# Kernel optimization log

Hardware: AMD Instinct MI355X
Metric: run time of the kernel (lower is better)

Reference implementation:

```python
import jax, jax.numpy as jnp
import numpy as np

DIM = 512
HEADS = 8
DHEAD = 64
INNER = HEADS * DHEAD
GAMMA = 0.01
LAMBDA_REG = 0.001


def _ln(x, g, b, eps=1e-5):
    mu = x.mean(-1, keepdims=True)
    var = jnp.var(x, axis=-1, keepdims=True)
    return (x - mu) / jnp.sqrt(var + eps) * g + b


def setup_inputs() -> dict:
    key = jax.random.key(0)
    ks = jax.random.split(key, 16)
    B, NQ, NK = 4, 1024, 1024
    s = 0.02
    return {
        "q": jax.random.normal(ks[0], (B, NQ, DIM), jnp.float32),
        "k": jax.random.normal(ks[1], (B, NK, DIM), jnp.float32),
        "v": jax.random.normal(ks[2], (B, NK, DIM), jnp.float32),
        "ln_g": jnp.ones((DIM,), jnp.float32),
        "ln_b": jnp.zeros((DIM,), jnp.float32),
        "W_in": jax.random.normal(ks[3], (DIM, INNER), jnp.float32) * s,
        "wp_W1": jax.random.normal(ks[4], (2 * DHEAD, 3 * DHEAD), jnp.float32) * s,
        "wp_b1": jnp.zeros((3 * DHEAD,), jnp.float32),
        "wp_lng": jnp.ones((3 * DHEAD,), jnp.float32),
        "wp_lnb": jnp.zeros((3 * DHEAD,), jnp.float32),
        "wp_W2": jax.random.normal(ks[5], (3 * DHEAD, 2 * DHEAD), jnp.float32) * s,
        "wp_b2": jnp.zeros((2 * DHEAD,), jnp.float32),
        "wp_W3": jax.random.normal(ks[6], (2 * DHEAD, 3), jnp.float32) * s,
        "wp_b3": jnp.zeros((3,), jnp.float32),
        "w_temp": jnp.array(1.8, jnp.float32),
        "W_out": jax.random.normal(ks[7], (INNER, DIM), jnp.float32) * s,
        "b_out": jnp.zeros((DIM,), jnp.float32),
    }


def _forward(q, k, v, ln_g, ln_b, W_in, wp_W1, wp_b1, wp_lng, wp_lnb,
             wp_W2, wp_b2, wp_W3, wp_b3, w_temp, W_out, b_out):
    h, d = HEADS, DHEAD
    sg = jax.lax.stop_gradient

    def proj(x):
        f = _ln(x, ln_g, ln_b) @ W_in               # [B,N,inner] (dropout: eval)
        B, N, _ = f.shape
        return f.reshape(B, N, h, d).transpose(2, 0, 1, 3)  # [h,B,N,d]

    f_q, f_k, f_v = proj(q), proj(k), proj(v)
    m = f_k.shape[2]
    eps = 1e-8

    # --- cosine_distance(f_q, f_k^T), clamped twice in original ---
    dots0 = jnp.einsum('hbnd,hbmd->hbnm', f_q, f_k)
    n1 = jnp.linalg.norm(f_q, axis=-1, keepdims=True) + eps      # [h,B,N,1]
    n2 = jnp.linalg.norm(f_k, axis=-1, keepdims=True) + eps      # [h,B,M,1]
    cosine_sim = jnp.clip(dots0 / (n1 * n2.transpose(0, 1, 3, 2)), -0.98, 0.98)

    # --- regularized covariance component ---
    f_k_c = f_k - f_k.mean(axis=2, keepdims=True)
    f_q_c = f_q - f_q.mean(axis=-1, keepdims=True)
    cov = jnp.einsum('hbnd,hbmd->hbnm', f_q_c, f_k_c) / (d ** 0.5 + 1e-6)
    health = sg(jnp.std(cov, ddof=1))
    base = LAMBDA_REG / m
    reg = jnp.where(health < 1e-5, base * 8.0,
                    jnp.where(health < 1e-3, base * 3.0, base))
    cov = jnp.clip(reg * cov, -30.0, 30.0)

    # --- margin-based variance component (eval: adaptive_gamma = gamma) ---
    fq_n = f_q / jnp.maximum(jnp.linalg.norm(f_q, axis=-1, keepdims=True), 1e-6)
    fk_n = f_k / jnp.maximum(jnp.linalg.norm(f_k, axis=-1, keepdims=True), 1e-6)
    cs = jnp.clip(jnp.einsum('hbnd,hbmd->hbnm', fq_n, fk_n), -0.98, 0.98)
    margin = jnp.clip(GAMMA - cs, 0.0, 8.0)
    var_c = jnp.broadcast_to(margin.mean(-1, keepdims=True), cs.shape)

    # --- dynamic per-head weights ---
    feat = jnp.concatenate([f_q.mean(axis=(1, 2)), f_k.mean(axis=(1, 2))], -1)  # [h,2d]
    hid = jax.nn.relu(_ln(feat @ wp_W1 + wp_b1, wp_lng, wp_lnb))
    hid = jax.nn.relu(hid @ wp_W2 + wp_b2)
    probs = jax.nn.softmax(hid @ wp_W3 + wp_b3, axis=-1)   # predictor ends in softmax
    wt = jnp.clip(w_temp, 0.05, 3.0)
    w = jax.nn.softmax(probs / wt, axis=-1)                # second softmax, per original
    w = jnp.clip(w, 0.05, 0.85)
    w = w / w.sum(-1, keepdims=True)
    cw = w[:, 0][:, None, None, None]
    covw = w[:, 1][:, None, None, None]
    varw = w[:, 2][:, None, None, None]

    cos_norm = sg(jnp.std(cosine_sim, ddof=1)) + 1e-6
    cov_norm = sg(jnp.std(cov, ddof=1)) + 1e-6
    var_norm = sg(jnp.std(var_c, ddof=1)) + 1e-6
    cos_h = jnp.minimum(cos_norm, 1.2)
    cov_h = jnp.minimum(cov_norm * 12.0, 1.2)
    var_h = jnp.minimum(var_norm * 12.0, 1.2)

    dots = (cw * (cosine_sim / cos_norm * cos_h)
            + covw * (cov / cov_norm * 0.5 * cov_h)
            + varw * (var_c / var_norm * 0.5 * var_h))

    div = sg(jnp.std(dots, ddof=1))
    temp = jnp.where(div < 5e-6, 0.03, jnp.where(div < 5e-4, 0.15, 0.4))
    attn = jax.nn.softmax(dots / temp, axis=-1)
    out = jnp.einsum('hbnm,hbmd->hbnd', attn, f_v)
    out = out.transpose(1, 2, 0, 3).reshape(q.shape[0], q.shape[1], h * d)
    return out @ W_out + b_out


def reference(q, k, v, ln_g, ln_b, W_in, wp_W1, wp_b1, wp_lng, wp_lnb,
              wp_W2, wp_b2, wp_W3, wp_b3, w_temp, W_out, b_out):
    return _forward(q, k, v, ln_g, ln_b, W_in, wp_W1, wp_b1, wp_lng, wp_lnb,
                    wp_W2, wp_b2, wp_W3, wp_b3, w_temp, W_out, b_out)
```

## Files before the change

### kernel.cpp

```cpp
#include <hip/hip_runtime.h>
#include <math.h>

#define SZ 2097152

typedef __attribute__((ext_vector_type(8))) short bf16x8;
typedef __attribute__((ext_vector_type(4))) float f32x4;
#define MFMA16(A,B,C) __builtin_amdgcn_mfma_f32_16x16x32_bf16(A,B,C,0,0,0)

__device__ __forceinline__ unsigned short f2b(float x) {
  unsigned int u = __float_as_uint(x);
  u = (u + 0x7fffu + ((u >> 16) & 1u)) >> 16;
  return (unsigned short)u;
}
__device__ __forceinline__ unsigned int pk2(float a, float b) {
  return (unsigned int)f2b(a) | ((unsigned int)f2b(b) << 16);
}
#define B2FL(u) __uint_as_float(((unsigned)(u)) << 16)
#define B2FH(u) __uint_as_float(((unsigned)(u)) & 0xffff0000u)

__device__ __forceinline__ float wredsum(float v) {
  #pragma unroll
  for (int o = 32; o; o >>= 1) v += __shfl_xor(v, o);
  return v;
}

__device__ __forceinline__ int swz(int r, int c) { return (r << 6) + ((c ^ (r & 7)) << 3); }

__device__ __forceinline__ bf16x8 ldfrag(const unsigned short* s, int row, int chunk) {
  return *reinterpret_cast<const bf16x8*>(&s[swz(row, chunk)]);
}

__device__ __forceinline__ void gl16(const unsigned short* g, unsigned short* l) {
  __builtin_amdgcn_global_load_lds(
      (const __attribute__((address_space(1))) void*)g,
      (__attribute__((address_space(3))) void*)l, 16, 0, 0);
}

__global__ __launch_bounds__(256) void k_pre(
    const float* __restrict__ q, const float* __restrict__ k, const float* __restrict__ v,
    const float* __restrict__ ln_g, const float* __restrict__ ln_b,
    const float* __restrict__ Win, const float* __restrict__ Wout,
    unsigned short* __restrict__ A_bf, unsigned short* __restrict__ WT,
    double* __restrict__ stats)
{
  __shared__ float t[64][65];
  const int bx = blockIdx.x;
  const int tid = threadIdx.x;
  if (bx < 128) {
    const int x = bx & 63;
    const int k0 = (x & 7) << 6, n0 = (x >> 3) << 6;
    const float* W = (bx >> 6) ? Wout : Win;
    unsigned short* dst = WT + (size_t)(bx >> 6) * 262144;
    for (int u = tid; u < 4096; u += 256) {
      const int r = u >> 6, c = u & 63;
      t[c][r] = W[(size_t)(k0 + r) * 512 + n0 + c];
    }
    __syncthreads();
    for (int u = tid; u < 4096; u += 256) {
      const int r = u >> 6, c = u & 63;
      dst[(size_t)(n0 + r) * 512 + k0 + c] = f2b(t[r][c]);
    }
    return;
  }
  if (bx == 3200) {
    if (tid < 72) stats[tid] = 0.0;
    return;
  }
  const int wv = tid >> 6, lane = tid & 63;
  const int row = (bx - 128) * 4 + wv;
  const int tt = row >> 12, g = row & 4095;
  const float* x = (tt == 0) ? q : (tt == 1) ? k : v;
  const float4* xr = reinterpret_cast<const float4*>(x + (size_t)g * 512);
  const float4 a0 = xr[2 * lane], a1 = xr[2 * lane + 1];
  float s  = a0.x + a0.y + a0.z + a0.w + a1.x + a1.y + a1.z + a1.w;
  float ss = a0.x*a0.x + a0.y*a0.y + a0.z*a0.z + a0.w*a0.w
           + a1.x*a1.x + a1.y*a1.y + a1.z*a1.z + a1.w*a1.w;
  #pragma unroll
  for (int o = 32; o; o >>= 1) { s += __shfl_xor(s, o); ss += __shfl_xor(ss, o); }
  const float mu = s * (1.f / 512.f);
  const float rstd = rsqrtf(ss * (1.f / 512.f) - mu * mu + 1e-5f);
  const float4* gg = reinterpret_cast<const float4*>(ln_g);
  const float4* bb = reinterpret_cast<const float4*>(ln_b);
  const float4 g0 = gg[2 * lane], g1 = gg[2 * lane + 1];
  const float4 b0 = bb[2 * lane], b1 = bb[2 * lane + 1];
  uint4 o4;
  o4.x = pk2((a0.x - mu) * rstd * g0.x + b0.x, (a0.y - mu) * rstd * g0.y + b0.y);
  o4.y = pk2((a0.z - mu) * rstd * g0.z + b0.z, (a0.w - mu) * rstd * g0.w + b0.w);
  o4.z = pk2((a1.x - mu) * rstd * g1.x + b1.x, (a1.y - mu) * rstd * g1.y + b1.y);
  o4.w = pk2((a1.z - mu) * rstd * g1.z + b1.z, (a1.w - mu) * rstd * g1.w + b1.w);
  *reinterpret_cast<uint4*>(&A_bf[(size_t)row * 512 + lane * 8]) = o4;
}

__global__ __launch_bounds__(256) void k_projcol(
    const unsigned short* __restrict__ A_bf, const unsigned short* __restrict__ WT,
    unsigned short* __restrict__ BF, float* __restrict__ partialA)
{
  __shared__ __align__(16) unsigned short smem[12288];
  const int tid = threadIdx.x;
  if (blockIdx.x >= 192) {
    const int u0 = (blockIdx.x - 192) * 4 + blockIdx.y;
    const int t = u0 >> 6, seg = u0 & 63;
    const unsigned int* src = reinterpret_cast<const unsigned int*>(
        A_bf + ((size_t)t * 4096 + seg * 64) * 512);
    float s0 = 0.f, s1 = 0.f;
    #pragma unroll 4
    for (int r = 0; r < 64; ++r) {
      const unsigned int vv = src[r * 256 + tid];
      s0 += B2FL(vv);
      s1 += B2FH(vv);
    }
    partialA[(((size_t)t * 64 + seg) << 9) + tid * 2] = s0;
    partialA[(((size_t)t * 64 + seg) << 9) + tid * 2 + 1] = s1;
    return;
  }
  unsigned short* As = smem;
  unsigned short* Bs = smem + 4096;
  const int m0 = blockIdx.x * 64;
  const int n0b = blockIdx.y * 128;
  const int w = tid >> 6, lane = tid & 63;
  const int wm = w >> 1, wn = w & 1;
  const int lr = lane & 15, lg = lane >> 4;
  f32x4 acc[2][4];
  #pragma unroll
  for (int mi = 0; mi < 2; ++mi)
    #pragma unroll
    for (int ni = 0; ni < 4; ++ni) acc[mi][ni] = f32x4{0.f, 0.f, 0.f, 0.f};

  for (int k0 = 0; k0 < 512; k0 += 64) {
    __syncthreads();
    #pragma unroll
    for (int p = 0; p < 2; ++p) {
      const int u = p * 256 + w * 64 + lane;
      const int r = u >> 3, cs = (u & 7) ^ (r & 7);
      gl16(&A_bf[(size_t)(m0 + r) * 512 + k0 + cs * 8], &As[(size_t)u * 8]);
    }
    #pragma unroll
    for (int p = 0; p < 4; ++p) {
      const int u = p * 256 + w * 64 + lane;
      const int r = u >> 3, cs = (u & 7) ^ (r & 7);
      gl16(&WT[(size_t)(n0b + r) * 512 + k0 + cs * 8], &Bs[(size_t)u * 8]);
    }
    __syncthreads();
    bf16x8 a[2][2];
    #pragma unroll
    for (int mi = 0; mi < 2; ++mi) {
      const int ar = wm * 32 + mi * 16 + lr;
      a[mi][0] = ldfrag(As, ar, lg);
      a[mi][1] = ldfrag(As, ar, 4 + lg);
    }
    #pragma unroll
    for (int ni = 0; ni < 4; ++ni) {
      const int br = wn * 64 + ni * 16 + lr;
      const bf16x8 b0 = ldfrag(Bs, br, lg);
      const bf16x8 b1 = ldfrag(Bs, br, 4 + lg);
      acc[0][ni] = MFMA16(a[0][0], b0, acc[0][ni]);
      acc[0][ni] = MFMA16(a[0][1], b1, acc[0][ni]);
      acc[1][ni] = MFMA16(a[1][0], b0, acc[1][ni]);
      acc[1][ni] = MFMA16(a[1][1], b1, acc[1][ni]);
    }
  }
  const int t = m0 >> 12;
  const int gmb = (m0 & 4095) + wm * 32;
  const int h = 2 * blockIdx.y + wn;
  if (t < 2) {
    #pragma unroll
    for (int mi = 0; mi < 2; ++mi) {
      #pragma unroll
      for (int reg = 0; reg < 4; ++reg) {
        float ss = 0.f;
        #pragma unroll
        for (int ni = 0; ni < 4; ++ni) { const float vv = acc[mi][ni][reg]; ss += vv * vv; }
        #pragma unroll
        for (int o = 1; o < 16; o <<= 1) ss += __shfl_xor(ss, o);
        const float inv = 1.f / (sqrtf(ss) + 1e-8f);
        const int g = gmb + mi * 16 + lg * 4 + reg;
        const int b = g >> 10, n = g & 1023;
        const size_t base = (size_t)t * SZ + ((((size_t)(h * 4 + b) << 10) | n) << 6);
        #pragma unroll
        for (int ni = 0; ni < 4; ++ni) {
          BF[base + ni * 16 + lr] = f2b(acc[mi][ni][reg] * inv);
        }
      }
    }
  } else {
    unsigned short* FVT = BF + (size_t)2 * SZ;
    __syncthreads();
    #pragma unroll
    for (int mi = 0; mi < 2; ++mi)
      #pragma unroll
      for (int ni = 0; ni < 4; ++ni)
        #pragma unroll
        for (int reg = 0; reg < 4; ++reg)
          smem[(wn * 64 + ni * 16 + lr) * 66 + (wm * 32 + mi * 16 + lg * 4 + reg)] =
              f2b(acc[mi][ni][reg]);
    __syncthreads();
    const int gv0 = m0 & 4095;
    const int b = gv0 >> 10, nb = gv0 & 1023;
    for (int u = tid; u < 4096; u += 256) {
      const int jl = u >> 5, nl = (u & 31) << 1;
      const int h2 = 2 * blockIdx.y + (jl >> 6), d = jl & 63;
      const unsigned int vv = *reinterpret_cast<const unsigned int*>(&smem[jl * 66 + nl]);
      *reinterpret_cast<unsigned int*>(
          &FVT[((size_t)(h2 * 4 + b) << 16) + d * 1024 + nb + nl]) = vv;
    }
  }
}

__global__ __launch_bounds__(256) void k_mid(const unsigned short* __restrict__ BF,
                                             const float* __restrict__ partialA,
                                             const unsigned short* __restrict__ WT,
                                             double* __restrict__ stats,
                                             float* __restrict__ feats)
{
  __shared__ __align__(16) unsigned short kn_s[4096];
  __shared__ float part[5][4];
  __shared__ float mean_s[512];
  const int tid = threadIdx.x;
  if (blockIdx.x >= 32) {
    const int t = blockIdx.x - 32;
    float a0 = 0.f, a1 = 0.f;
    #pragma unroll 8
    for (int s = 0; s < 64; ++s) {
      a0 += partialA[(((size_t)t * 64 + s) << 9) + tid * 2];
      a1 += partialA[(((size_t)t * 64 + s) << 9) + tid * 2 + 1];
    }
    mean_s[tid * 2] = a0 * (1.f / 4096.f);
    mean_s[tid * 2 + 1] = a1 * (1.f / 4096.f);
    __syncthreads();
    #pragma unroll
    for (int uu = 0; uu < 2; ++uu) {
      const int j = tid * 2 + uu;
      const unsigned short* wr = WT + (size_t)j * 512;
      float a = 0.f;
      for (int kk = 0; kk < 512; ++kk) a += mean_s[kk] * B2FL(wr[kk]);
      feats[t * 512 + j] = a;
    }
    return;
  }
  const int pair = blockIdx.x, h = pair >> 2;
  const int w = tid >> 6, lane = tid & 63;
  const int lr = lane & 15, lg = lane >> 4;
  const size_t pb = (size_t)pair * 65536;
  const unsigned short* fqn = BF + pb;
  const unsigned short* fkn = BF + (size_t)SZ + pb;

  const int qrow = w * 16 + lr;
  const unsigned short* qnp = fqn + (size_t)qrow * 64;
  const bf16x8 qn0 = *reinterpret_cast<const bf16x8*>(qnp + lg * 8);
  const bf16x8 qn1 = *reinterpret_cast<const bf16x8*>(qnp + 32 + lg * 8);

  float sx = 0.f, sxx = 0.f;
  float rxs[4] = {0, 0, 0, 0}, rms[4] = {0, 0, 0, 0};

  for (int m0 = 0; m0 < 1024; m0 += 64) {
    __syncthreads();
    #pragma unroll
    for (int p = 0; p < 2; ++p) {
      const int u = p * 256 + w * 64 + lane;
      const int r = u >> 3, cs = (u & 7) ^ (r & 7);
      gl16(&fkn[((size_t)(m0 + r) << 6) + cs * 8], &kn_s[(size_t)u * 8]);
    }
    __syncthreads();
    #pragma unroll
    for (int nt = 0; nt < 4; ++nt) {
      const int krow = nt * 16 + lr;
      f32x4 dn = {0.f, 0.f, 0.f, 0.f};
      dn = MFMA16(qn0, ldfrag(kn_s, krow, lg), dn);
      dn = MFMA16(qn1, ldfrag(kn_s, krow, 4 + lg), dn);
      #pragma unroll
      for (int r = 0; r < 4; ++r) {
        const float X = fminf(fmaxf(dn[r], -0.98f), 0.98f);
        sx += X; sxx += X * X;
        rxs[r] += X; rms[r] += fmaxf(0.01f - X, 0.f);
      }
    }
  }
  const float g0 = wredsum(sx), g1 = wredsum(sxx);
  #pragma unroll
  for (int r = 0; r < 4; ++r) {
    #pragma unroll
    for (int o = 1; o < 16; o <<= 1) {
      rxs[r] += __shfl_xor(rxs[r], o);
      rms[r] += __shfl_xor(rms[r], o);
    }
  }
  float z1 = 0.f, z2 = 0.f, z3 = 0.f;
  if (lr == 0) {
    #pragma unroll
    for (int r = 0; r < 4; ++r) {
      const float Z = rms[r] * (1.f / 1024.f);
      z1 += Z; z2 += Z * Z; z3 += Z * rxs[r];
    }
  }
  z1 = wredsum(z1); z2 = wredsum(z2); z3 = wredsum(z3);
  if (lane == 0) {
    part[0][w] = g0; part[1][w] = g1; part[2][w] = z1; part[3][w] = z2; part[4][w] = z3;
  }
  __syncthreads();
  if (tid == 0) {
    const int dst[5] = {0, 1, 5, 6, 7};
    #pragma unroll
    for (int i = 0; i < 5; ++i) {
      const double s = (double)part[i][0] + part[i][1] + part[i][2] + part[i][3];
      atomicAdd(&stats[h * 9 + dst[i]], s);
    }
  }
}

__global__ __launch_bounds__(512) void k_finalize(
    const float* __restrict__ feats, const double* __restrict__ stats,
    const float* __restrict__ W1, const float* __restrict__ b1,
    const float* __restrict__ lng, const float* __restrict__ lnb,
    const float* __restrict__ W2, const float* __restrict__ b2,
    const float* __restrict__ W3, const float* __restrict__ b3,
    const float* __restrict__ w_temp, float* __restrict__ coefs)
{
  __shared__ float feat[8][128];
  __shared__ float h1[8][192];
  __shared__ float y2[8][128];
  __shared__ float wsm[8][3];
  const int tid = threadIdx.x;
  const int h = tid >> 6, lane = tid & 63;

  feat[h][lane] = feats[h * 64 + lane];
  feat[h][64 + lane] = feats[512 + h * 64 + lane];
  float y1v[3];
  {
    float a0 = b1[lane], a1 = b1[lane + 64], a2 = b1[lane + 128];
    for (int i = 0; i < 128; ++i) {
      const float fv = feat[h][i];
      const float* wr = W1 + (size_t)i * 192;
      a0 += fv * wr[lane];
      a1 += fv * wr[lane + 64];
      a2 += fv * wr[lane + 128];
    }
    y1v[0] = a0; y1v[1] = a1; y1v[2] = a2;
  }
  float s = y1v[0] + y1v[1] + y1v[2];
  float ss = y1v[0]*y1v[0] + y1v[1]*y1v[1] + y1v[2]*y1v[2];
  s = wredsum(s); ss = wredsum(ss);
  const float mu = s * (1.f / 192.f);
  const float rstd = rsqrtf(ss * (1.f / 192.f) - mu * mu + 1e-5f);
  #pragma unroll
  for (int u = 0; u < 3; ++u) {
    const int j = lane + u * 64;
    h1[h][j] = fmaxf((y1v[u] - mu) * rstd * lng[j] + lnb[j], 0.f);
  }
  {
    float a0 = b2[lane], a1 = b2[lane + 64];
    for (int i = 0; i < 192; ++i) {
      const float hv = h1[h][i];
      const float* wr = W2 + (size_t)i * 128;
      a0 += hv * wr[lane];
      a1 += hv * wr[lane + 64];
    }
    y2[h][lane] = fmaxf(a0, 0.f);
    y2[h][lane + 64] = fmaxf(a1, 0.f);
  }
  {
    float l0, l1, l2;
    const float va = y2[h][lane], vb = y2[h][lane + 64];
    const float* wa = W3 + (size_t)lane * 3;
    const float* wb = W3 + (size_t)(lane + 64) * 3;
    l0 = va * wa[0] + vb * wb[0];
    l1 = va * wa[1] + vb * wb[1];
    l2 = va * wa[2] + vb * wb[2];
    l0 = wredsum(l0); l1 = wredsum(l1); l2 = wredsum(l2);
    if (lane == 0) {
      l0 += b3[0]; l1 += b3[1]; l2 += b3[2];
      float mx = fmaxf(l0, fmaxf(l1, l2));
      float e0 = expf(l0 - mx), e1 = expf(l1 - mx), e2 = expf(l2 - mx);
      float se = e0 + e1 + e2;
      const float p0 = e0 / se, p1 = e1 / se, p2 = e2 / se;
      const float wt = fminf(fmaxf(w_temp[0], 0.05f), 3.f);
      const float q0 = p0 / wt, q1 = p1 / wt, q2 = p2 / wt;
      mx = fmaxf(q0, fmaxf(q1, q2));
      e0 = expf(q0 - mx); e1 = expf(q1 - mx); e2 = expf(q2 - mx);
      se = e0 + e1 + e2;
      float w0 = e0 / se, w1 = e1 / se, w2 = e2 / se;
      w0 = fminf(fmaxf(w0, 0.05f), 0.85f);
      w1 = fminf(fmaxf(w1, 0.05f), 0.85f);
      w2 = fminf(fmaxf(w2, 0.05f), 0.85f);
      const float swt = w0 + w1 + w2;
      wsm[h][0] = w0 / swt; wsm[h][1] = w1 / swt; wsm[h][2] = w2 / swt;
    }
  }
  __syncthreads();
  if (tid == 0) {
    const double n = 2097152.0, M = 1024.0;
    const double L2E = 1.4426950408889634;
    double S[8][9], T[9];
    for (int i = 0; i < 9; ++i) T[i] = 0.0;
    for (int hh = 0; hh < 8; ++hh)
      for (int i = 0; i < 9; ++i) { S[hh][i] = stats[hh * 9 + i]; T[i] += S[hh][i]; }
    const double cos_norm = sqrt(fmax((T[1] - T[0] * T[0] / n) / (n - 1.0), 0.0)) + 1e-6;
    const double zvar = (M * T[6] - (M * T[5]) * (M * T[5]) / n) / (n - 1.0);
    const double var_norm = sqrt(fmax(zvar, 0.0)) + 1e-6;
    const double cos_h = fmin(cos_norm, 1.2);
    const double var_h = fmin(var_norm * 12.0, 1.2);
    double D1 = 0.0, D2 = 0.0, Ah[8];
    for (int hh = 0; hh < 8; ++hh) {
      const double A = (double)wsm[hh][0] * cos_h / cos_norm;
      const double C = (double)wsm[hh][2] * 0.5 * var_h / var_norm;
      Ah[hh] = A;
      D1 += A * S[hh][0] + C * M * S[hh][5];
      D2 += A * A * S[hh][1] + C * C * M * S[hh][6] + 2.0 * A * C * S[hh][7];
    }
    const double divv = sqrt(fmax((D2 - D1 * D1 / n) / (n - 1.0), 0.0));
    const double temp = (divv < 5e-6) ? 0.03 : ((divv < 5e-4) ? 0.15 : 0.4);
    for (int hh = 0; hh < 8; ++hh) {
      const float Pp = (float)(Ah[hh] / temp * L2E);
      coefs[hh] = Pp;
      coefs[16 + hh] = fabsf(Pp) * 0.98f;
    }
  }
}

__global__ __launch_bounds__(256) void k_attn(const unsigned short* __restrict__ BF,
                                              const float* __restrict__ coefs,
                                              unsigned short* __restrict__ po,
                                              float* __restrict__ pl)
{
  __shared__ __align__(16) unsigned short kn_s[4096], vt_s[4096], P_s[4096];
  const int pair = blockIdx.y, h = pair >> 2, seg = blockIdx.z;
  const int r0 = blockIdx.x * 64;
  const int tid = threadIdx.x;
  const int w = tid >> 6, lane = tid & 63;
  const int lr = lane & 15, lg = lane >> 4;
  const size_t pb = (size_t)pair * 65536;
  const unsigned short* fqn = BF + pb;
  const unsigned short* fkn = BF + (size_t)SZ + pb;
  const unsigned short* fvt = BF + (size_t)2 * SZ + pb;
  const float P = coefs[h], MB = coefs[16 + h];

  const int qrow = r0 + w * 16 + lr;
  const unsigned short* qnp = fqn + (size_t)qrow * 64;
  const bf16x8 qn0 = *reinterpret_cast<const bf16x8*>(qnp + lg * 8);
  const bf16x8 qn1 = *reinterpret_cast<const bf16x8*>(qnp + 32 + lg * 8);

  float lsum = 0.f;
  f32x4 o[4];
  #pragma unroll
  for (int i = 0; i < 4; ++i) o[i] = f32x4{0.f, 0.f, 0.f, 0.f};

  const int qb = w * 16 + lr;
  const int pofs = 4 * (lg & 1);
  const int chi = lg >> 1;

  const int mbeg = seg << 9;
  for (int m0 = mbeg; m0 < mbeg + 512; m0 += 64) {
    __syncthreads();
    #pragma unroll
    for (int p = 0; p < 2; ++p) {
      const int u = p * 256 + w * 64 + lane;
      const int r = u >> 3, cs = (u & 7) ^ (r & 7);
      gl16(&fkn[((size_t)(m0 + r) << 6) + cs * 8], &kn_s[(size_t)u * 8]);
      gl16(&fvt[(size_t)r * 1024 + m0 + cs * 8], &vt_s[(size_t)u * 8]);
    }
    __syncthreads();

    __builtin_amdgcn_s_setprio(1);
    #pragma unroll
    for (int nt = 0; nt < 4; ++nt) {
      const int krow = nt * 16 + lr;
      f32x4 dn = {0.f, 0.f, 0.f, 0.f};
      dn = MFMA16(ldfrag(kn_s, krow, lg), qn0, dn);
      dn = MFMA16(ldfrag(kn_s, krow, 4 + lg), qn1, dn);
      float e[4];
      #pragma unroll
      for (int r = 0; r < 4; ++r) {
        const float X = fminf(fmaxf(dn[r], -0.98f), 0.98f);
        e[r] = exp2f(P * X - MB);
        lsum += e[r];
      }
      unsigned int w0, w1;
      asm("v_cvt_pk_bf16_f32 %0, %1, %2" : "=v"(w0) : "v"(e[0]), "v"(e[1]));
      asm("v_cvt_pk_bf16_f32 %0, %1, %2" : "=v"(w1) : "v"(e[2]), "v"(e[3]));
      const int chunk = 2 * nt + chi;
      *reinterpret_cast<uint2*>(
          &P_s[(qb << 6) + ((chunk ^ (qb & 7)) << 3) + pofs]) = uint2{w0, w1};
    }
    const int parow = w * 16 + lr;
    const bf16x8 pa0 = ldfrag(P_s, parow, lg);
    const bf16x8 pa1 = ldfrag(P_s, parow, 4 + lg);
    #pragma unroll
    for (int nt2 = 0; nt2 < 4; ++nt2) {
      const int vrow = nt2 * 16 + lr;
      o[nt2] = MFMA16(pa0, ldfrag(vt_s, vrow, lg), o[nt2]);
      o[nt2] = MFMA16(pa1, ldfrag(vt_s, vrow, 4 + lg), o[nt2]);
    }
    __builtin_amdgcn_s_setprio(0);
  }
  lsum += __shfl_xor(lsum, 16);
  lsum += __shfl_xor(lsum, 32);
  const size_t sb = (size_t)seg * SZ;
  #pragma unroll
  for (int r = 0; r < 4; ++r) {
    const int lrow = w * 16 + 4 * lg + r;
    const size_t orow = sb + pb + ((size_t)(r0 + lrow) << 6);
    #pragma unroll
    for (int nt2 = 0; nt2 < 4; ++nt2) {
      po[orow + nt2 * 16 + lr] = f2b(o[nt2][r]);
    }
  }
  if (lg == 0) {
    pl[(seg << 15) + pair * 1024 + r0 + w * 16 + lr] = lsum;
  }
}

__global__ __launch_bounds__(256) void k_gemm_out(
    const unsigned short* __restrict__ po, const float* __restrict__ pl,
    const unsigned short* __restrict__ WT,
    const float* __restrict__ bias, float* __restrict__ out)
{
  __shared__ __align__(16) unsigned short As[2048], Bs[8192];
  __shared__ float sinv_s[256];
  const int m0 = blockIdx.x * 32;
  const int n0b = blockIdx.y * 128;
  const int tid = threadIdx.x;
  const int w = tid >> 6, lane = tid & 63;
  const int wm = w >> 1, wn = w & 1;
  const int lr = lane & 15, lg = lane >> 4;
  {
    const int r2 = tid >> 3, h2 = tid & 7;
    const int g2 = m0 + r2;
    const int rowid = (h2 * 4 + (g2 >> 10)) * 1024 + (g2 & 1023);
    sinv_s[tid] = 1.f / (pl[rowid] + pl[32768 + rowid]);
  }
  f32x4 acc[4];
  #pragma unroll
  for (int ni = 0; ni < 4; ++ni) acc[ni] = f32x4{0.f, 0.f, 0.f, 0.f};

  for (int k0 = 0; k0 < 512; k0 += 64) {
    __syncthreads();
    {
      const int r = tid >> 3, c = tid & 7;
      const int g = m0 + r;
      const int j0 = k0 + c * 8;
      const int h = k0 >> 6;
      const size_t base = ((size_t)(h * 4 + (g >> 10)) << 16) + ((size_t)(g & 1023) << 6) + (j0 & 63);
      const uint4 v0 = *reinterpret_cast<const uint4*>(po + base);
      const uint4 v1 = *reinterpret_cast<const uint4*>(po + (size_t)SZ + base);
      const float sv = sinv_s[r * 8 + h];
      uint4 o4;
      o4.x = pk2((B2FL(v0.x) + B2FL(v1.x)) * sv, (B2FH(v0.x) + B2FH(v1.x)) * sv);
      o4.y = pk2((B2FL(v0.y) + B2FL(v1.y)) * sv, (B2FH(v0.y) + B2FH(v1.y)) * sv);
      o4.z = pk2((B2FL(v0.z) + B2FL(v1.z)) * sv, (B2FH(v0.z) + B2FH(v1.z)) * sv);
      o4.w = pk2((B2FL(v0.w) + B2FL(v1.w)) * sv, (B2FH(v0.w) + B2FH(v1.w)) * sv);
      *reinterpret_cast<uint4*>(&As[swz(r, c)]) = o4;
    }
    #pragma unroll
    for (int p = 0; p < 4; ++p) {
      const int u = p * 256 + w * 64 + lane;
      const int r = u >> 3, cs = (u & 7) ^ (r & 7);
      gl16(&WT[(size_t)(n0b + r) * 512 + k0 + cs * 8], &Bs[(size_t)u * 8]);
    }
    __syncthreads();
    const int ar = wm * 16 + lr;
    const bf16x8 a0 = ldfrag(As, ar, lg);
    const bf16x8 a1 = ldfrag(As, ar, 4 + lg);
    #pragma unroll
    for (int ni = 0; ni < 4; ++ni) {
      const int br = wn * 64 + ni * 16 + lr;
      const bf16x8 b0 = ldfrag(Bs, br, lg);
      const bf16x8 b1 = ldfrag(Bs, br, 4 + lg);
      acc[ni] = MFMA16(a0, b0, acc[ni]);
      acc[ni] = MFMA16(a1, b1, acc[ni]);
    }
  }
  #pragma unroll
  for (int ni = 0; ni < 4; ++ni) {
    const int j = n0b + wn * 64 + ni * 16 + lr;
    const float bj = bias[j];
    #pragma unroll
    for (int reg = 0; reg < 4; ++reg) {
      const int g = m0 + wm * 16 + lg * 4 + reg;
      out[(size_t)g * 512 + j] = acc[ni][reg] + bj;
    }
  }
}

extern "C" void kernel_launch(void* const* d_in, const int* in_sizes, int n_in,
                              void* d_out, int out_size, void* d_ws, size_t ws_size,
                              hipStream_t stream) {
  (void)in_sizes; (void)n_in; (void)out_size; (void)ws_size;
  const float* q      = (const float*)d_in[0];
  const float* k      = (const float*)d_in[1];
  const float* v      = (const float*)d_in[2];
  const float* ln_g   = (const float*)d_in[3];
  const float* ln_b   = (const float*)d_in[4];
  const float* W_in   = (const float*)d_in[5];
  const float* wp_W1  = (const float*)d_in[6];
  const float* wp_b1  = (const float*)d_in[7];
  const float* wp_lng = (const float*)d_in[8];
  const float* wp_lnb = (const float*)d_in[9];
  const float* wp_W2  = (const float*)d_in[10];
  const float* wp_b2  = (const float*)d_in[11];
  const float* wp_W3  = (const float*)d_in[12];
  const float* wp_b3  = (const float*)d_in[13];
  const float* w_temp = (const float*)d_in[14];
  const float* W_out  = (const float*)d_in[15];
  const float* b_out  = (const float*)d_in[16];

  float* ws = (float*)d_ws;
  unsigned short* BF = (unsigned short*)ws;
  unsigned short* A_bf = BF + (size_t)3 * SZ;
  unsigned short* po = (unsigned short*)(ws + (size_t)3 * SZ / 2);
  float* AUX  = ws + (size_t)13631488;
  float* feats  = AUX;
  float* coefs = AUX + 4096;
  double* stats = (double*)(AUX + 4160);
  unsigned short* WT = (unsigned short*)(AUX + 8192);
  float* partialA = AUX + 270336;
  float* pl = AUX + 8192;

  k_pre<<<3201, 256, 0, stream>>>(q, k, v, ln_g, ln_b, W_in, W_out, A_bf, WT, stats);
  k_projcol<<<dim3(224, 4), 256, 0, stream>>>(A_bf, WT, BF, partialA);
  k_mid<<<34, 256, 0, stream>>>(BF, partialA, WT, stats, feats);
  k_finalize<<<1, 512, 0, stream>>>(feats, stats, wp_W1, wp_b1, wp_lng, wp_lnb,
                                    wp_W2, wp_b2, wp_W3, wp_b3, w_temp, coefs);
  k_attn<<<dim3(16, 32, 2), 256, 0, stream>>>(BF, coefs, po, pl);
  k_gemm_out<<<dim3(128, 4), 256, 0, stream>>>(po, pl, WT + 262144, b_out, (float*)d_out);
}
```

Before: 95.91 us.

## Double-buffer LDS tiles in projection, attention and output GEMM kernels

Result: slower. 100.5 us (+4.8%).

```diff
diff --git a/kernel.cpp b/kernel.cpp
--- a/kernel.cpp
+++ b/kernel.cpp
@@ -95,7 +95,7 @@
     const unsigned short* __restrict__ A_bf, const unsigned short* __restrict__ WT,
     unsigned short* __restrict__ BF, float* __restrict__ partialA)
 {
-  __shared__ __align__(16) unsigned short smem[12288];
+  __shared__ __align__(16) unsigned short smem[24576];
   const int tid = threadIdx.x;
   if (blockIdx.x >= 192) {
     const int u0 = (blockIdx.x - 192) * 4 + blockIdx.y;
@@ -113,8 +113,6 @@
     partialA[(((size_t)t * 64 + seg) << 9) + tid * 2 + 1] = s1;
     return;
   }
-  unsigned short* As = smem;
-  unsigned short* Bs = smem + 4096;
   const int m0 = blockIdx.x * 64;
   const int n0b = blockIdx.y * 128;
   const int w = tid >> 6, lane = tid & 63;
@@ -126,21 +124,41 @@
     #pragma unroll
     for (int ni = 0; ni < 4; ++ni) acc[mi][ni] = f32x4{0.f, 0.f, 0.f, 0.f};
 
-  for (int k0 = 0; k0 < 512; k0 += 64) {
-    __syncthreads();
-    #pragma unroll
-    for (int p = 0; p < 2; ++p) {
-      const int u = p * 256 + w * 64 + lane;
-      const int r = u >> 3, cs = (u & 7) ^ (r & 7);
-      gl16(&A_bf[(size_t)(m0 + r) * 512 + k0 + cs * 8], &As[(size_t)u * 8]);
-    }
-    #pragma unroll
-    for (int p = 0; p < 4; ++p) {
-      const int u = p * 256 + w * 64 + lane;
-      const int r = u >> 3, cs = (u & 7) ^ (r & 7);
-      gl16(&WT[(size_t)(n0b + r) * 512 + k0 + cs * 8], &Bs[(size_t)u * 8]);
-    }
-    __syncthreads();
+  #pragma unroll
+  for (int p = 0; p < 2; ++p) {
+    const int u = p * 256 + w * 64 + lane;
+    const int r = u >> 3, cs = (u & 7) ^ (r & 7);
+    gl16(&A_bf[(size_t)(m0 + r) * 512 + cs * 8], &smem[(size_t)u * 8]);
+  }
+  #pragma unroll
+  for (int p = 0; p < 4; ++p) {
+    const int u = p * 256 + w * 64 + lane;
+    const int r = u >> 3, cs = (u & 7) ^ (r & 7);
+    gl16(&WT[(size_t)(n0b + r) * 512 + cs * 8], &smem[8192 + (size_t)u * 8]);
+  }
+  __syncthreads();
+  int cur = 0;
+  for (int kt = 0; kt < 8; ++kt) {
+    if (kt < 7) {
+      const int k0 = (kt + 1) * 64;
+      const int nb = (cur ^ 1);
+      #pragma unroll
+      for (int p = 0; p < 2; ++p) {
+        const int u = p * 256 + w * 64 + lane;
+        const int r = u >> 3, cs = (u & 7) ^ (r & 7);
+        gl16(&A_bf[(size_t)(m0 + r) * 512 + k0 + cs * 8],
+             &smem[nb * 4096 + (size_t)u * 8]);
+      }
+      #pragma unroll
+      for (int p = 0; p < 4; ++p) {
+        const int u = p * 256 + w * 64 + lane;
+        const int r = u >> 3, cs = (u & 7) ^ (r & 7);
+        gl16(&WT[(size_t)(n0b + r) * 512 + k0 + cs * 8],
+             &smem[8192 + nb * 8192 + (size_t)u * 8]);
+      }
+    }
+    const unsigned short* As = smem + cur * 4096;
+    const unsigned short* Bs = smem + 8192 + cur * 8192;
     bf16x8 a[2][2];
     #pragma unroll
     for (int mi = 0; mi < 2; ++mi) {
@@ -148,6 +166,7 @@
       a[mi][0] = ldfrag(As, ar, lg);
       a[mi][1] = ldfrag(As, ar, 4 + lg);
     }
+    __builtin_amdgcn_s_setprio(1);
     #pragma unroll
     for (int ni = 0; ni < 4; ++ni) {
       const int br = wn * 64 + ni * 16 + lr;
@@ -158,6 +177,9 @@
       acc[1][ni] = MFMA16(a[1][0], b0, acc[1][ni]);
       acc[1][ni] = MFMA16(a[1][1], b1, acc[1][ni]);
     }
+    __builtin_amdgcn_s_setprio(0);
+    __syncthreads();
+    cur ^= 1;
   }
   const int t = m0 >> 12;
   const int gmb = (m0 & 4095) + wm * 32;
@@ -184,7 +206,6 @@
     }
   } else {
     unsigned short* FVT = BF + (size_t)2 * SZ;
-    __syncthreads();
     #pragma unroll
     for (int mi = 0; mi < 2; ++mi)
       #pragma unroll
@@ -421,7 +442,7 @@
                                               unsigned short* __restrict__ po,
                                               float* __restrict__ pl)
 {
-  __shared__ __align__(16) unsigned short kn_s[4096], vt_s[4096], P_s[4096];
+  __shared__ __align__(16) unsigned short kn_s[2][4096], vt_s[2][4096], P_s[4096];
   const int pair = blockIdx.y, h = pair >> 2, seg = blockIdx.z;
   const int r0 = blockIdx.x * 64;
   const int tid = threadIdx.x;
@@ -446,26 +467,37 @@
   const int qb = w * 16 + lr;
   const int pofs = 4 * (lg & 1);
   const int chi = lg >> 1;
-
   const int mbeg = seg << 9;
-  for (int m0 = mbeg; m0 < mbeg + 512; m0 += 64) {
-    __syncthreads();
-    #pragma unroll
-    for (int p = 0; p < 2; ++p) {
-      const int u = p * 256 + w * 64 + lane;
-      const int r = u >> 3, cs = (u & 7) ^ (r & 7);
-      gl16(&fkn[((size_t)(m0 + r) << 6) + cs * 8], &kn_s[(size_t)u * 8]);
-      gl16(&fvt[(size_t)r * 1024 + m0 + cs * 8], &vt_s[(size_t)u * 8]);
-    }
-    __syncthreads();
-
+
+  #pragma unroll
+  for (int p = 0; p < 2; ++p) {
+    const int u = p * 256 + w * 64 + lane;
+    const int r = u >> 3, cs = (u & 7) ^ (r & 7);
+    gl16(&fkn[((size_t)(mbeg + r) << 6) + cs * 8], &kn_s[0][(size_t)u * 8]);
+    gl16(&fvt[(size_t)r * 1024 + mbeg + cs * 8], &vt_s[0][(size_t)u * 8]);
+  }
+  __syncthreads();
+  int cur = 0;
+  for (int ti = 0; ti < 8; ++ti) {
+    if (ti < 7) {
+      const int m0 = mbeg + (ti + 1) * 64;
+      #pragma unroll
+      for (int p = 0; p < 2; ++p) {
+        const int u = p * 256 + w * 64 + lane;
+        const int r = u >> 3, cs = (u & 7) ^ (r & 7);
+        gl16(&fkn[((size_t)(m0 + r) << 6) + cs * 8], &kn_s[cur ^ 1][(size_t)u * 8]);
+        gl16(&fvt[(size_t)r * 1024 + m0 + cs * 8], &vt_s[cur ^ 1][(size_t)u * 8]);
+      }
+    }
+    const unsigned short* kc = kn_s[cur];
+    const unsigned short* vc = vt_s[cur];
     __builtin_amdgcn_s_setprio(1);
     #pragma unroll
     for (int nt = 0; nt < 4; ++nt) {
       const int krow = nt * 16 + lr;
       f32x4 dn = {0.f, 0.f, 0.f, 0.f};
-      dn = MFMA16(ldfrag(kn_s, krow, lg), qn0, dn);
-      dn = MFMA16(ldfrag(kn_s, krow, 4 + lg), qn1, dn);
+      dn = MFMA16(ldfrag(kc, krow, lg), qn0, dn);
+      dn = MFMA16(ldfrag(kc, krow, 4 + lg), qn1, dn);
       float e[4];
       #pragma unroll
       for (int r = 0; r < 4; ++r) {
@@ -486,10 +518,12 @@
     #pragma unroll
     for (int nt2 = 0; nt2 < 4; ++nt2) {
       const int vrow = nt2 * 16 + lr;
-      o[nt2] = MFMA16(pa0, ldfrag(vt_s, vrow, lg), o[nt2]);
-      o[nt2] = MFMA16(pa1, ldfrag(vt_s, vrow, 4 + lg), o[nt2]);
+      o[nt2] = MFMA16(pa0, ldfrag(vc, vrow, lg), o[nt2]);
+      o[nt2] = MFMA16(pa1, ldfrag(vc, vrow, 4 + lg), o[nt2]);
     }
     __builtin_amdgcn_s_setprio(0);
+    __syncthreads();
+    cur ^= 1;
   }
   lsum += __shfl_xor(lsum, 16);
   lsum += __shfl_xor(lsum, 32);
@@ -513,7 +547,7 @@
     const unsigned short* __restrict__ WT,
     const float* __restrict__ bias, float* __restrict__ out)
 {
-  __shared__ __align__(16) unsigned short As[2048], Bs[8192];
+  __shared__ __align__(16) unsigned short As[2][2048], Bs[2][8192];
   __shared__ float sinv_s[256];
   const int m0 = blockIdx.x * 32;
   const int n0b = blockIdx.y * 128;
@@ -527,46 +561,74 @@
     const int rowid = (h2 * 4 + (g2 >> 10)) * 1024 + (g2 & 1023);
     sinv_s[tid] = 1.f / (pl[rowid] + pl[32768 + rowid]);
   }
+  __syncthreads();
   f32x4 acc[4];
   #pragma unroll
   for (int ni = 0; ni < 4; ++ni) acc[ni] = f32x4{0.f, 0.f, 0.f, 0.f};
 
-  for (int k0 = 0; k0 < 512; k0 += 64) {
-    __syncthreads();
-    {
-      const int r = tid >> 3, c = tid & 7;
-      const int g = m0 + r;
-      const int j0 = k0 + c * 8;
+  const int ra = tid >> 3, ca = tid & 7;
+  const int ga = m0 + ra;
+
+  {
+    const int j0 = ca * 8;
+    const size_t ab = ((size_t)(ga >> 10) << 16) + ((size_t)(ga & 1023) << 6) + (j0 & 63);
+    const uint4 v0 = *reinterpret_cast<const uint4*>(po + ab);
+    const uint4 v1 = *reinterpret_cast<const uint4*>(po + (size_t)SZ + ab);
+    const float sv = sinv_s[ra * 8 + 0];
+    uint4 o4;
+    o4.x = pk2((B2FL(v0.x) + B2FL(v1.x)) * sv, (B2FH(v0.x) + B2FH(v1.x)) * sv);
+    o4.y = pk2((B2FL(v0.y) + B2FL(v1.y)) * sv, (B2FH(v0.y) + B2FH(v1.y)) * sv);
+    o4.z = pk2((B2FL(v0.z) + B2FL(v1.z)) * sv, (B2FH(v0.z) + B2FH(v1.z)) * sv);
+    o4.w = pk2((B2FL(v0.w) + B2FL(v1.w)) * sv, (B2FH(v0.w) + B2FH(v1.w)) * sv);
+    *reinterpret_cast<uint4*>(&As[0][swz(ra, ca)]) = o4;
+    #pragma unroll
+    for (int p = 0; p < 4; ++p) {
+      const int u = p * 256 + w * 64 + lane;
+      const int r = u >> 3, cs = (u & 7) ^ (r & 7);
+      gl16(&WT[(size_t)(n0b + r) * 512 + cs * 8], &Bs[0][(size_t)u * 8]);
+    }
+  }
+  __syncthreads();
+  int cur = 0;
+  for (int kt = 0; kt < 8; ++kt) {
+    if (kt < 7) {
+      const int k0 = (kt + 1) * 64;
+      const int j0 = k0 + ca * 8;
       const int h = k0 >> 6;
-      const size_t base = ((size_t)(h * 4 + (g >> 10)) << 16) + ((size_t)(g & 1023) << 6) + (j0 & 63);
-      const uint4 v0 = *reinterpret_cast<const uint4*>(po + base);
-      const uint4 v1 = *reinterpret_cast<const uint4*>(po + (size_t)SZ + base);
-      const float sv = sinv_s[r * 8 + h];
+      const size_t ab = ((size_t)(h * 4 + (ga >> 10)) << 16) + ((size_t)(ga & 1023) << 6) + (j0 & 63);
+      const uint4 v0 = *reinterpret_cast<const uint4*>(po + ab);
+      const uint4 v1 = *reinterpret_cast<const uint4*>(po + (size_t)SZ + ab);
+      const float sv = sinv_s[ra * 8 + h];
       uint4 o4;
       o4.x = pk2((B2FL(v0.x) + B2FL(v1.x)) * sv, (B2FH(v0.x) + B2FH(v1.x)) * sv);
       o4.y = pk2((B2FL(v0.y) + B2FL(v1.y)) * sv, (B2FH(v0.y) + B2FH(v1.y)) * sv);
       o4.z = pk2((B2FL(v0.z) + B2FL(v1.z)) * sv, (B2FH(v0.z) + B2FH(v1.z)) * sv);
       o4.w = pk2((B2FL(v0.w) + B2FL(v1.w)) * sv, (B2FH(v0.w) + B2FH(v1.w)) * sv);
-      *reinterpret_cast<uint4*>(&As[swz(r, c)]) = o4;
-    }
-    #pragma unroll
-    for (int p = 0; p < 4; ++p) {
-      const int u = p * 256 + w * 64 + lane;
-      const int r = u >> 3, cs = (u & 7) ^ (r & 7);
-      gl16(&WT[(size_t)(n0b + r) * 512 + k0 + cs * 8], &Bs[(size_t)u * 8]);
-    }
-    __syncthreads();
+      *reinterpret_cast<uint4*>(&As[cur ^ 1][swz(ra, ca)]) = o4;
+      #pragma unroll
+      for (int p = 0; p < 4; ++p) {
+        const int u = p * 256 + w * 64 + lane;
+        const int r = u >> 3, cs = (u & 7) ^ (r & 7);
+        gl16(&WT[(size_t)(n0b + r) * 512 + k0 + cs * 8], &Bs[cur ^ 1][(size_t)u * 8]);
+      }
+    }
+    const unsigned short* Ac = As[cur];
+    const unsigned short* Bc = Bs[cur];
     const int ar = wm * 16 + lr;
-    const bf16x8 a0 = ldfrag(As, ar, lg);
-    const bf16x8 a1 = ldfrag(As, ar, 4 + lg);
+    const bf16x8 a0 = ldfrag(Ac, ar, lg);
+    const bf16x8 a1 = ldfrag(Ac, ar, 4 + lg);
+    __builtin_amdgcn_s_setprio(1);
     #pragma unroll
     for (int ni = 0; ni < 4; ++ni) {
       const int br = wn * 64 + ni * 16 + lr;
-      const bf16x8 b0 = ldfrag(Bs, br, lg);
-      const bf16x8 b1 = ldfrag(Bs, br, 4 + lg);
+      const bf16x8 b0 = ldfrag(Bc, br, lg);
+      const bf16x8 b1 = ldfrag(Bc, br, 4 + lg);
       acc[ni] = MFMA16(a0, b0, acc[ni]);
       acc[ni] = MFMA16(a1, b1, acc[ni]);
     }
+    __builtin_amdgcn_s_setprio(0);
+    __syncthreads();
+    cur ^= 1;
   }
   #pragma unroll
   for (int ni = 0; ni < 4; ++ni) {
```
